# Kernel tuning notes

Hardware: AMD Instinct MI355X
Metric: run time of the kernel (lower is better)

## Reference

```python
import jax, jax.numpy as jnp
import numpy as np

VOCAB = 50257
W_DIM = 1024   # embedding / input width (config.n_embd)
H_DIM = 1024   # LSTM hidden size
NUM_CLASSES = 2
B, T = 32, 2048


def setup_inputs() -> dict:
    key = jax.random.key(0)
    ks = jax.random.split(key, 7)
    s = 0.02
    seq = jax.random.randint(ks[0], (B, T), 0, VOCAB)
    emb = jax.random.normal(ks[1], (VOCAB, W_DIM), dtype=jnp.float32) * s
    W_ih = jax.random.normal(ks[2], (4 * H_DIM, W_DIM), dtype=jnp.float32) * s
    W_hh = jax.random.normal(ks[3], (4 * H_DIM, H_DIM), dtype=jnp.float32) * s
    b_ih = jax.random.normal(ks[4], (4 * H_DIM,), dtype=jnp.float32) * s
    b_hh = jax.random.normal(ks[5], (4 * H_DIM,), dtype=jnp.float32) * s
    W_score = jax.random.normal(ks[6], (NUM_CLASSES, H_DIM), dtype=jnp.float32) * s
    return {"seq": seq, "emb": emb, "W_ih": W_ih, "W_hh": W_hh,
            "b_ih": b_ih, "b_hh": b_hh, "W_score": W_score}


def _lstm_scan(x_gates, W_hh):
    # x_gates: [T, B, 4H] = precomputed input contribution + biases
    H = W_hh.shape[1]
    h0 = jnp.zeros((x_gates.shape[1], H), dtype=x_gates.dtype)
    c0 = jnp.zeros_like(h0)

    def step(carry, xg):
        h, c = carry
        gates = xg + h @ W_hh.T                 # [B, 4H]
        i, f, g, o = jnp.split(gates, 4, axis=-1)  # PyTorch LSTMCell gate order
        i = jax.nn.sigmoid(i)
        f = jax.nn.sigmoid(f)
        g = jnp.tanh(g)
        o = jax.nn.sigmoid(o)
        c = f * c + i * g
        h = o * jnp.tanh(c)
        return (h, c), h

    _, hs = jax.lax.scan(step, (h0, c0), x_gates)  # hs: [T, B, H]
    return hs


def reference(seq, emb, W_ih, W_hh, b_ih, b_hh, W_score):
    # fudge=True: return per-timestep logits [B, T, num_classes]. Dropout in eval mode (identity).
    x = emb[seq]                                      # [B, T, W]
    x_gates = jnp.einsum('btw,gw->btg', x, W_ih) + b_ih + b_hh  # [B, T, 4H]
    hs = _lstm_scan(x_gates.transpose(1, 0, 2), W_hh)           # [T, B, H]
    h = hs.transpose(1, 0, 2)                         # [B, T, H]
    out = jnp.maximum(h, 0.0) @ W_score.T             # score_net: ReLU -> Linear(no bias)
    return out
```

## Files before the change

### kernel.cpp

```cpp
#include <hip/hip_runtime.h>
#include <hip/hip_bf16.h>


typedef _Float16 f16;
typedef _Float16 f16x8 __attribute__((ext_vector_type(8)));
typedef _Float16 f16x4 __attribute__((ext_vector_type(4)));
typedef float    f32x4 __attribute__((ext_vector_type(4)));
typedef unsigned long long u64;

#define B_    32
#define T_    2048
#define H_    1024
#define G4_   4096

__device__ __forceinline__ void gl_lds16(const void* g, void* l) {
  __builtin_amdgcn_global_load_lds(
      (const __attribute__((address_space(1))) void*)g,
      (__attribute__((address_space(3))) void*)l, 16, 0, 0);
}

__device__ __forceinline__ void llc_st64(void* p, u64 v) {
  __hip_atomic_store((u64*)p, v, __ATOMIC_RELAXED, __HIP_MEMORY_SCOPE_AGENT);
}

__device__ __forceinline__ float fast_sigmoid(float v) {
  return __builtin_amdgcn_rcpf(1.f + __expf(-v));
}
__device__ __forceinline__ float fast_tanh(float v) {
  return 1.f - 2.f * __builtin_amdgcn_rcpf(1.f + __expf(2.f * v));
}


__global__ void k_cvt_f16(const float* __restrict__ in, f16* __restrict__ out, long n4) {
  long i = (long)blockIdx.x * blockDim.x + threadIdx.x;
  if (i >= n4) return;
  float4 v = ((const float4*)in)[i];
  f16x4 o; o[0] = (f16)v.x; o[1] = (f16)v.y; o[2] = (f16)v.z; o[3] = (f16)v.w;
  *(f16x4*)(out + i * 4) = o;
}

__global__ void k_whh_reorder(const float* __restrict__ whh, f16* __restrict__ wr) {
  unsigned i = blockIdx.x * blockDim.x + threadIdx.x;
  unsigned e0 = i * 8;
  unsigned R = e0 >> 10, k = e0 & 1023;
  unsigned q = R >> 10, j = R & 1023;
  unsigned outR = ((j >> 4) << 6) + ((j & 15) << 2) + q;
  float4 v0 = ((const float4*)whh)[e0 / 4];
  float4 v1 = ((const float4*)whh)[e0 / 4 + 1];
  f16x8 o;
  o[0] = (f16)v0.x; o[1] = (f16)v0.y; o[2] = (f16)v0.z; o[3] = (f16)v0.w;
  o[4] = (f16)v1.x; o[5] = (f16)v1.y; o[6] = (f16)v1.z; o[7] = (f16)v1.w;
  *(f16x8*)&wr[((size_t)outR << 10) + k] = o;
}

__global__ void k_bias(const float* __restrict__ bi, const float* __restrict__ bh,
                       float* __restrict__ bo) {
  unsigned i = blockIdx.x * blockDim.x + threadIdx.x;
  if (i < G4_) bo[i] = bi[i] + bh[i];
}


__global__ __launch_bounds__(256) void k_gemm_xg(
    const int* __restrict__ seq, const f16* __restrict__ emb16,
    const f16* __restrict__ wih16, const float* __restrict__ bias,
    f16* __restrict__ xg) {
  __shared__ f16 As[128 * 64];
  __shared__ f16 Bs[128 * 64];
  const unsigned tid = threadIdx.x;
  const unsigned w = tid >> 6, lane = tid & 63;
  const unsigned bid = blockIdx.x;
  const unsigned tn = bid & 31, tm = bid >> 5;
  const unsigned wm = (w >> 1) * 64, wn = (w & 1) * 64;

  f32x4 zero = {0.f, 0.f, 0.f, 0.f};
  f32x4 acc[4][4];
#pragma unroll
  for (int i = 0; i < 4; ++i)
#pragma unroll
    for (int j = 0; j < 4; ++j) acc[i][j] = zero;

  for (unsigned kk = 0; kk < 16; ++kk) {
    const unsigned k0 = kk * 64;
#pragma unroll
    for (unsigned c = 0; c < 4; ++c) {
      unsigned idx = c * 256 + tid;
      unsigned row = idx >> 3, ch = idx & 7;
      unsigned chs = ch ^ (row & 7);
      unsigned m = tm * 128 + row;
      unsigned t = m >> 5, b = m & 31;
      int e = seq[b * 2048 + t];
      const f16* src = emb16 + ((size_t)e << 10) + k0 + chs * 8;
      gl_lds16(src, (char*)As + c * 4096 + w * 1024);
    }
#pragma unroll
    for (unsigned c = 0; c < 4; ++c) {
      unsigned idx = c * 256 + tid;
      unsigned row = idx >> 3, ch = idx & 7;
      unsigned chs = ch ^ (row & 7);
      unsigned n = tn * 128 + row;
      const f16* src = wih16 + ((size_t)n << 10) + k0 + chs * 8;
      gl_lds16(src, (char*)Bs + c * 4096 + w * 1024);
    }
    __syncthreads();
#pragma unroll
    for (unsigned ks = 0; ks < 2; ++ks) {
      f16x8 af[4], bf[4];
      unsigned kc = ks * 4 + (lane >> 4);
#pragma unroll
      for (unsigned fm = 0; fm < 4; ++fm) {
        unsigned r = wm + fm * 16 + (lane & 15);
        af[fm] = *(const f16x8*)&As[r * 64 + ((kc ^ (r & 7)) << 3)];
      }
#pragma unroll
      for (unsigned fn = 0; fn < 4; ++fn) {
        unsigned r = wn + fn * 16 + (lane & 15);
        bf[fn] = *(const f16x8*)&Bs[r * 64 + ((kc ^ (r & 7)) << 3)];
      }
#pragma unroll
      for (unsigned fm = 0; fm < 4; ++fm)
#pragma unroll
        for (unsigned fn = 0; fn < 4; ++fn)
          acc[fm][fn] = __builtin_amdgcn_mfma_f32_16x16x32_f16(af[fm], bf[fn], acc[fm][fn], 0, 0, 0);
    }
    __syncthreads();
  }
#pragma unroll
  for (unsigned fn = 0; fn < 4; ++fn) {
    unsigned n = tn * 128 + wn + fn * 16 + (lane & 15);
    unsigned q = n >> 10, j = n & 1023;
    unsigned Rp = ((j >> 4) << 6) + ((j & 15) << 2) + q;
    float bv = bias[n];
#pragma unroll
    for (unsigned fm = 0; fm < 4; ++fm) {
#pragma unroll
      for (unsigned rg = 0; rg < 4; ++rg) {
        unsigned m = tm * 128 + wm + fm * 16 + (lane >> 4) * 4 + rg;
        xg[(size_t)m * G4_ + Rp] = (f16)(acc[fm][fn][rg] + bv);
      }
    }
  }
}


__global__ __launch_bounds__(256) void k_lstm(
    const f16* __restrict__ xg, const f16* __restrict__ wr16,
    f16* __restrict__ h_all) {
  __shared__ f16 Wl[64 * 512];
  __shared__ f16 Hl[2][16 * 1024];
  const unsigned tid = threadIdx.x;
  const unsigned nt = tid >> 6, lane = tid & 63;
  const unsigned wid = blockIdx.x;
  const unsigned rl = lane & 15, hi = lane >> 4;

  for (unsigned c = 0; c < 16; ++c) {
    unsigned idx = c * 256 + tid;
    unsigned row = idx >> 6, ch = idx & 63;
    unsigned chs = ch ^ (row & 7);
    const f16* src = wr16 + (((size_t)wid * 64 + row) << 10) + chs * 8;
    gl_lds16(src, (char*)Wl + c * 4096 + nt * 1024);
  }

  const unsigned rWl = nt * 16 + rl;
  f16x8 breg[16];
  {
    const f16* wp = wr16 + (((size_t)wid * 64 + rWl) << 10) + 512 + hi * 8;
#pragma unroll
    for (int j = 0; j < 16; ++j) {
      asm volatile("global_load_dwordx4 %0, %1, off\n\ts_waitcnt vmcnt(0)"
                   : "=v"(breg[j]) : "v"(wp + j * 32) : "memory");
    }
  }
  __syncthreads();

  const unsigned srow = tid >> 4;
  const unsigned scg = (tid & 15) * 8;
  float cA = 0.f, cB = 0.f;
  f16x8 st[8];
  f16x4 xvA, xvB;

  {
    const f16* gp0 = h_all + ((size_t)srow) * H_ + scg * 8;
#pragma unroll
    for (int j = 0; j < 8; ++j)
      asm volatile("global_load_dwordx4 %0, %1, off sc0 sc1"
                   : "=v"(st[j]) : "v"(gp0 + j * 8) : "memory");
    const f16* xp = xg + ((size_t)rl) * G4_ + wid * 64 + (nt * 4 + hi) * 4;
    asm volatile("global_load_dwordx2 %0, %1, off"
                 : "=v"(xvA) : "v"(xp) : "memory");
    if (hi == 0) {
      llc_st64(h_all + ((size_t)rl) * H_ + wid * 16 + nt * 4, 0ull);
    }
  }

  for (unsigned t = 1; t <= (unsigned)T_; ++t) {
#pragma unroll
    for (int s = 0; s < 2; ++s) {
      const unsigned sb16 = s * 16;
      const unsigned pb = ((t - 1) * 2 + s) & 1;
      const f16* gp = h_all + ((size_t)(t - 1) * B_ + sb16 + srow) * H_ + scg * 8;
      asm volatile("s_waitcnt vmcnt(2)" ::: "memory");
      __builtin_amdgcn_sched_barrier(0);
      while (true) {
        bool ok = true;
#pragma unroll
        for (int j = 0; j < 8; ++j) {
          union { f16x8 v; u64 u[2]; } uu; uu.v = st[j];
          ok = ok && (uu.u[0] != ~0ull) && (uu.u[1] != ~0ull);
        }
        if (ok) break;
        __builtin_amdgcn_s_sleep(1);
#pragma unroll
        for (int j = 0; j < 8; ++j)
          asm volatile("global_load_dwordx4 %0, %1, off sc0 sc1"
                       : "=v"(st[j]) : "v"(gp + j * 8) : "memory");
        asm volatile("s_waitcnt vmcnt(0)" ::: "memory");
        __builtin_amdgcn_sched_barrier(0);
      }
#pragma unroll
      for (int j = 0; j < 8; ++j) {
        unsigned cc = scg + j;
        unsigned pos = cc ^ (srow & 7) ^ ((cc >> 3) & 7);
        *(f16x8*)&Hl[pb][srow * 1024 + (pos << 3)] = st[j];
      }
      asm volatile("s_waitcnt lgkmcnt(0)" ::: "memory");
      __builtin_amdgcn_sched_barrier(0);
      __builtin_amdgcn_s_barrier();

      f32x4 acc0 = {0.f, 0.f, 0.f, 0.f};
      f32x4 acc1 = {0.f, 0.f, 0.f, 0.f};
#pragma unroll
      for (unsigned ks = 0; ks < 16; ks += 2) {
        unsigned c0 = ks * 4 + hi, c1 = c0 + 4;
        unsigned p0 = c0 ^ (rl & 7) ^ ((c0 >> 3) & 7);
        unsigned p1 = c1 ^ (rl & 7) ^ ((c1 >> 3) & 7);
        f16x8 h0 = *(const f16x8*)&Hl[pb][rl * 1024 + (p0 << 3)];
        f16x8 h1 = *(const f16x8*)&Hl[pb][rl * 1024 + (p1 << 3)];
        f16x8 w0 = *(const f16x8*)&Wl[rWl * 512 + ((c0 ^ (rWl & 7)) << 3)];
        f16x8 w1 = *(const f16x8*)&Wl[rWl * 512 + ((c1 ^ (rWl & 7)) << 3)];
        acc0 = __builtin_amdgcn_mfma_f32_16x16x32_f16(w0, h0, acc0, 0, 0, 0);
        acc1 = __builtin_amdgcn_mfma_f32_16x16x32_f16(w1, h1, acc1, 0, 0, 0);
      }
#pragma unroll
      for (unsigned ks = 16; ks < 32; ks += 2) {
        unsigned c0 = ks * 4 + hi, c1 = c0 + 4;
        unsigned p0 = c0 ^ (rl & 7) ^ ((c0 >> 3) & 7);
        unsigned p1 = c1 ^ (rl & 7) ^ ((c1 >> 3) & 7);
        f16x8 h0 = *(const f16x8*)&Hl[pb][rl * 1024 + (p0 << 3)];
        f16x8 h1 = *(const f16x8*)&Hl[pb][rl * 1024 + (p1 << 3)];
        acc0 = __builtin_amdgcn_mfma_f32_16x16x32_f16(breg[ks - 16], h0, acc0, 0, 0, 0);
        acc1 = __builtin_amdgcn_mfma_f32_16x16x32_f16(breg[ks - 15], h1, acc1, 0, 0, 0);
      }
      asm volatile("s_waitcnt vmcnt(1)" ::: "memory");
      __builtin_amdgcn_sched_barrier(0);
      f16x4 xv4 = (s == 0) ? xvA : xvB;

      unsigned nt_t = (s == 0) ? t : (t < (unsigned)T_ ? t + 1 : t);
      unsigned nsb = (s == 0) ? 16u : 0u;
      const f16* gpn = h_all + ((size_t)(nt_t - 1) * B_ + nsb + srow) * H_ + scg * 8;
#pragma unroll
      for (int j = 0; j < 8; ++j)
        asm volatile("global_load_dwordx4 %0, %1, off sc0 sc1"
                     : "=v"(st[j]) : "v"(gpn + j * 8) : "memory");
      {
        const f16* xpn = xg + ((size_t)(nt_t - 1) * B_ + nsb + rl) * G4_
                         + wid * 64 + (nt * 4 + hi) * 4;
        if (s == 0)
          asm volatile("global_load_dwordx2 %0, %1, off"
                       : "=v"(xvB) : "v"(xpn) : "memory");
        else
          asm volatile("global_load_dwordx2 %0, %1, off"
                       : "=v"(xvA) : "v"(xpn) : "memory");
      }

      {
        float gi = acc0[0] + acc1[0] + (float)xv4[0];
        float gf = acc0[1] + acc1[1] + (float)xv4[1];
        float gg = acc0[2] + acc1[2] + (float)xv4[2];
        float go = acc0[3] + acc1[3] + (float)xv4[3];
        float i_ = fast_sigmoid(gi);
        float f_ = fast_sigmoid(gf);
        float g_ = fast_tanh(gg);
        float o_ = fast_sigmoid(go);
        float c_ = (s == 0) ? cA : cB;
        c_ = f_ * c_ + i_ * g_;
        if (s == 0) cA = c_; else cB = c_;
        float hv = o_ * fast_tanh(c_);
        float h1v = __shfl(hv, (int)(rl + 16), 64);
        float h2v = __shfl(hv, (int)(rl + 32), 64);
        float h3v = __shfl(hv, (int)(rl + 48), 64);
        if (hi == 0) {
          union { f16 h4[4]; u64 u; } pk;
          pk.h4[0] = (f16)hv;  pk.h4[1] = (f16)h1v;
          pk.h4[2] = (f16)h2v; pk.h4[3] = (f16)h3v;
          llc_st64(h_all + ((size_t)t * B_ + sb16 + rl) * H_ + wid * 16 + nt * 4,
                   pk.u);
        }
      }
    }
  }
}


__global__ __launch_bounds__(256) void k_logits(
    const f16* __restrict__ h_all, const float* __restrict__ wsc,
    float* __restrict__ out) {
  __shared__ float Ws[2048];
  unsigned tid = threadIdx.x;
  for (unsigned i = tid; i < 512; i += 256) ((float4*)Ws)[i] = ((const float4*)wsc)[i];
  __syncthreads();
  unsigned w = tid >> 6, lane = tid & 63;
  unsigned base = blockIdx.x * 64 + w * 16;
  for (unsigned i = 0; i < 16; ++i) {
    unsigned idx = base + i;
    unsigned tt = idx >> 5, b = idx & 31;
    const f16* hp = h_all + ((size_t)(idx + 32)) * H_ + lane * 16;
    f16x8 ha = *(const f16x8*)hp;
    f16x8 hb = *(const f16x8*)(hp + 8);
    float s0 = 0.f, s1 = 0.f;
#pragma unroll
    for (int z = 0; z < 8; ++z) {
      float hv = fmaxf((float)ha[z], 0.f);
      s0 += hv * Ws[lane * 16 + z];
      s1 += hv * Ws[1024 + lane * 16 + z];
    }
#pragma unroll
    for (int z = 0; z < 8; ++z) {
      float hv = fmaxf((float)hb[z], 0.f);
      s0 += hv * Ws[lane * 16 + 8 + z];
      s1 += hv * Ws[1024 + lane * 16 + 8 + z];
    }
#pragma unroll
    for (int off = 32; off; off >>= 1) {
      s0 += __shfl_xor(s0, off, 64);
      s1 += __shfl_xor(s1, off, 64);
    }
    if (lane == 0) {
      out[((size_t)b * T_ + tt) * 2 + 0] = s0;
      out[((size_t)b * T_ + tt) * 2 + 1] = s1;
    }
  }
}


extern "C" void kernel_launch(void* const* d_in, const int* in_sizes, int n_in,
                              void* d_out, int out_size, void* d_ws, size_t ws_size,
                              hipStream_t stream) {
  const int*   seq = (const int*)d_in[0];
  const float* emb = (const float*)d_in[1];
  const float* wih = (const float*)d_in[2];
  const float* whh = (const float*)d_in[3];
  const float* bih = (const float*)d_in[4];
  const float* bhh = (const float*)d_in[5];
  const float* wsc = (const float*)d_in[6];
  float* out = (float*)d_out;
  char* ws = (char*)d_ws;

  const size_t NEED = 790874112ull;
  if (ws_size < NEED) return;

  f16*   emb16 = (f16*)(ws);
  f16*   wih16 = (f16*)(ws + 102926336ull);
  f16*   wr16  = (f16*)(ws + 111314944ull);
  float* bias  = (float*)(ws + 119703552ull);
  f16*   xg    = (f16*)(ws + 119719936ull);
  f16*   h_all = (f16*)(ws + 656590848ull);

  hipMemsetAsync(h_all, 0, (size_t)B_ * H_ * 2, stream);
  hipMemsetAsync((char*)h_all + (size_t)B_ * H_ * 2, 0xFF,
                 (size_t)T_ * B_ * H_ * 2, stream);

  k_cvt_f16<<<50257, 256, 0, stream>>>(emb, emb16, 12865792L);
  k_cvt_f16<<<4096, 256, 0, stream>>>(wih, wih16, 1048576L);
  k_whh_reorder<<<2048, 256, 0, stream>>>(whh, wr16);
  k_bias<<<16, 256, 0, stream>>>(bih, bhh, bias);

  k_gemm_xg<<<16384, 256, 0, stream>>>(seq, emb16, wih16, bias, xg);
  k_lstm<<<64, 256, 0, stream>>>(xg, wr16, h_all);
  k_logits<<<1024, 256, 0, stream>>>(h_all, wsc, out);
}
```

Baseline: 11.47 ms.

## Split LSTM recurrence batch into four 8-row sub-batches for finer pipelining

The persistent LSTM kernel now processes the 32-row batch as four sub-batches of 8 rows instead of two of 16. Each step loads half as much h data per thread and writes only 8 valid rows. The aim is a shorter dependency chain per sub-step, so one sub-batch's h exchange overlaps with computation on the others. The cost is that the 16-wide MFMA tiles run half empty (rows are duplicated via rl&7), and there are twice as many barriers and polling rounds per timestep.

```diff
diff --git a/kernel.cpp b/kernel.cpp
--- a/kernel.cpp
+++ b/kernel.cpp
@@ -146,7 +146,7 @@
     const f16* __restrict__ xg, const f16* __restrict__ wr16,
     f16* __restrict__ h_all) {
   __shared__ f16 Wl[64 * 512];
-  __shared__ f16 Hl[2][16 * 1024];
+  __shared__ f16 Hl[2][8 * 1024];
   const unsigned tid = threadIdx.x;
   const unsigned nt = tid >> 6, lane = tid & 63;
   const unsigned wid = blockIdx.x;
@@ -172,52 +172,53 @@
   }
   __syncthreads();
 
-  const unsigned srow = tid >> 4;
-  const unsigned scg = (tid & 15) * 8;
-  float cA = 0.f, cB = 0.f;
-  f16x8 st[8];
-  f16x4 xvA, xvB;
+  const unsigned srow = tid >> 5;
+  const unsigned scg = (tid & 31) * 4;
+  const unsigned rlc = rl & 7;
+  float cS[4] = {0.f, 0.f, 0.f, 0.f};
+  f16x8 st[4];
+  f16x4 xvS[4];
 
   {
     const f16* gp0 = h_all + ((size_t)srow) * H_ + scg * 8;
 #pragma unroll
-    for (int j = 0; j < 8; ++j)
+    for (int j = 0; j < 4; ++j)
       asm volatile("global_load_dwordx4 %0, %1, off sc0 sc1"
                    : "=v"(st[j]) : "v"(gp0 + j * 8) : "memory");
-    const f16* xp = xg + ((size_t)rl) * G4_ + wid * 64 + (nt * 4 + hi) * 4;
+    const f16* xp = xg + ((size_t)rlc) * G4_ + wid * 64 + (nt * 4 + hi) * 4;
     asm volatile("global_load_dwordx2 %0, %1, off"
-                 : "=v"(xvA) : "v"(xp) : "memory");
-    if (hi == 0) {
+                 : "=v"(xvS[0]) : "v"(xp) : "memory");
+    if (hi == 0 && rl < 8) {
       llc_st64(h_all + ((size_t)rl) * H_ + wid * 16 + nt * 4, 0ull);
     }
   }
 
   for (unsigned t = 1; t <= (unsigned)T_; ++t) {
 #pragma unroll
-    for (int s = 0; s < 2; ++s) {
-      const unsigned sb16 = s * 16;
-      const unsigned pb = ((t - 1) * 2 + s) & 1;
-      const f16* gp = h_all + ((size_t)(t - 1) * B_ + sb16 + srow) * H_ + scg * 8;
+    for (int s = 0; s < 4; ++s) {
+      const unsigned sb8 = s * 8;
+      const unsigned pb = ((t - 1) * 4 + s) & 1;
+      const f16* gp = h_all + ((size_t)(t - 1) * B_ + sb8 + srow) * H_ + scg * 8;
       asm volatile("s_waitcnt vmcnt(2)" ::: "memory");
       __builtin_amdgcn_sched_barrier(0);
       while (true) {
         bool ok = true;
 #pragma unroll
-        for (int j = 0; j < 8; ++j) {
+        for (int j = 0; j < 4; ++j) {
           union { f16x8 v; u64 u[2]; } uu; uu.v = st[j];
           ok = ok && (uu.u[0] != ~0ull) && (uu.u[1] != ~0ull);
         }
         if (ok) break;
         __builtin_amdgcn_s_sleep(1);
 #pragma unroll
-        for (int j = 0; j < 8; ++j)
+        for (int j = 0; j < 4; ++j)
           asm volatile("global_load_dwordx4 %0, %1, off sc0 sc1"
                        : "=v"(st[j]) : "v"(gp + j * 8) : "memory");
         asm volatile("s_waitcnt vmcnt(0)" ::: "memory");
         __builtin_amdgcn_sched_barrier(0);
       }
 #pragma unroll
-      for (int j = 0; j < 8; ++j) {
+      for (int j = 0; j < 4; ++j) {
         unsigned cc = scg + j;
         unsigned pos = cc ^ (srow & 7) ^ ((cc >> 3) & 7);
         *(f16x8*)&Hl[pb][srow * 1024 + (pos << 3)] = st[j];
@@ -231,10 +232,10 @@
 #pragma unroll
       for (unsigned ks = 0; ks < 16; ks += 2) {
         unsigned c0 = ks * 4 + hi, c1 = c0 + 4;
-        unsigned p0 = c0 ^ (rl & 7) ^ ((c0 >> 3) & 7);
-        unsigned p1 = c1 ^ (rl & 7) ^ ((c1 >> 3) & 7);
-        f16x8 h0 = *(const f16x8*)&Hl[pb][rl * 1024 + (p0 << 3)];
-        f16x8 h1 = *(const f16x8*)&Hl[pb][rl * 1024 + (p1 << 3)];
+        unsigned p0 = c0 ^ (rlc & 7) ^ ((c0 >> 3) & 7);
+        unsigned p1 = c1 ^ (rlc & 7) ^ ((c1 >> 3) & 7);
+        f16x8 h0 = *(const f16x8*)&Hl[pb][rlc * 1024 + (p0 << 3)];
+        f16x8 h1 = *(const f16x8*)&Hl[pb][rlc * 1024 + (p1 << 3)];
         f16x8 w0 = *(const f16x8*)&Wl[rWl * 512 + ((c0 ^ (rWl & 7)) << 3)];
         f16x8 w1 = *(const f16x8*)&Wl[rWl * 512 + ((c1 ^ (rWl & 7)) << 3)];
         acc0 = __builtin_amdgcn_mfma_f32_16x16x32_f16(w0, h0, acc0, 0, 0, 0);
@@ -243,33 +244,30 @@
 #pragma unroll
       for (unsigned ks = 16; ks < 32; ks += 2) {
         unsigned c0 = ks * 4 + hi, c1 = c0 + 4;
-        unsigned p0 = c0 ^ (rl & 7) ^ ((c0 >> 3) & 7);
-        unsigned p1 = c1 ^ (rl & 7) ^ ((c1 >> 3) & 7);
-        f16x8 h0 = *(const f16x8*)&Hl[pb][rl * 1024 + (p0 << 3)];
-        f16x8 h1 = *(const f16x8*)&Hl[pb][rl * 1024 + (p1 << 3)];
+        unsigned p0 = c0 ^ (rlc & 7) ^ ((c0 >> 3) & 7);
+        unsigned p1 = c1 ^ (rlc & 7) ^ ((c1 >> 3) & 7);
+        f16x8 h0 = *(const f16x8*)&Hl[pb][rlc * 1024 + (p0 << 3)];
+        f16x8 h1 = *(const f16x8*)&Hl[pb][rlc * 1024 + (p1 << 3)];
         acc0 = __builtin_amdgcn_mfma_f32_16x16x32_f16(breg[ks - 16], h0, acc0, 0, 0, 0);
         acc1 = __builtin_amdgcn_mfma_f32_16x16x32_f16(breg[ks - 15], h1, acc1, 0, 0, 0);
       }
       asm volatile("s_waitcnt vmcnt(1)" ::: "memory");
       __builtin_amdgcn_sched_barrier(0);
-      f16x4 xv4 = (s == 0) ? xvA : xvB;
-
-      unsigned nt_t = (s == 0) ? t : (t < (unsigned)T_ ? t + 1 : t);
-      unsigned nsb = (s == 0) ? 16u : 0u;
+      f16x4 xv4 = xvS[s];
+
+      unsigned nt_t = (s < 3) ? t : (t < (unsigned)T_ ? t + 1 : t);
+      unsigned nsb = (s < 3) ? (sb8 + 8) : 0u;
       const f16* gpn = h_all + ((size_t)(nt_t - 1) * B_ + nsb + srow) * H_ + scg * 8;
 #pragma unroll
-      for (int j = 0; j < 8; ++j)
+      for (int j = 0; j < 4; ++j)
         asm volatile("global_load_dwordx4 %0, %1, off sc0 sc1"
                      : "=v"(st[j]) : "v"(gpn + j * 8) : "memory");
       {
-        const f16* xpn = xg + ((size_t)(nt_t - 1) * B_ + nsb + rl) * G4_
+        const f16* xpn = xg + ((size_t)(nt_t - 1) * B_ + nsb + rlc) * G4_
                          + wid * 64 + (nt * 4 + hi) * 4;
-        if (s == 0)
-          asm volatile("global_load_dwordx2 %0, %1, off"
-                       : "=v"(xvB) : "v"(xpn) : "memory");
-        else
-          asm volatile("global_load_dwordx2 %0, %1, off"
-                       : "=v"(xvA) : "v"(xpn) : "memory");
+        f16x4* dst = &xvS[(s + 1) & 3];
+        asm volatile("global_load_dwordx2 %0, %1, off"
+                     : "=v"(*dst) : "v"(xpn) : "memory");
       }
 
       {
@@ -281,18 +279,18 @@
         float f_ = fast_sigmoid(gf);
         float g_ = fast_tanh(gg);
         float o_ = fast_sigmoid(go);
-        float c_ = (s == 0) ? cA : cB;
+        float c_ = cS[s];
         c_ = f_ * c_ + i_ * g_;
-        if (s == 0) cA = c_; else cB = c_;
+        cS[s] = c_;
         float hv = o_ * fast_tanh(c_);
         float h1v = __shfl(hv, (int)(rl + 16), 64);
         float h2v = __shfl(hv, (int)(rl + 32), 64);
         float h3v = __shfl(hv, (int)(rl + 48), 64);
-        if (hi == 0) {
+        if (hi == 0 && rl < 8) {
           union { f16 h4[4]; u64 u; } pk;
           pk.h4[0] = (f16)hv;  pk.h4[1] = (f16)h1v;
           pk.h4[2] = (f16)h2v; pk.h4[3] = (f16)h3v;
-          llc_st64(h_all + ((size_t)t * B_ + sb16 + rl) * H_ + wid * 16 + nt * 4,
+          llc_st64(h_all + ((size_t)t * B_ + sb8 + rl) * H_ + wid * 16 + nt * 4,
                    pk.u);
         }
       }
```

New measurement: 12.11 ms. 5.5% more time.
